# Performance work log

Hardware: AMD Instinct MI355X
Metric: run time of the kernel (lower is better)

The kernel has to match this reference:

```python
import jax, jax.numpy as jnp
import numpy as np

ACT_BITS = 8  # global_act_bit in the original repo
QMAX = float(2 ** ACT_BITS - 1)


def _fake_quant_asym(x):
    """Asymmetric per-tensor fake quantization (weight_quant_fn, activate=True)."""
    mx = jnp.max(x)
    mn = jnp.min(x)
    scale = (mx - mn) / QMAX
    zp = jnp.round(-mn / scale)
    q = jnp.clip(jnp.round(x / scale) + zp, 0.0, QMAX)
    return (q - zp) * scale


def setup_inputs() -> dict:
    key = jax.random.key(0)
    kx, kq, kr, kl, ks = jax.random.split(key, 5)
    B, S, IN, OUT, R = 32, 1024, 1152, 1152, 64
    x = jax.random.normal(kx, (B, S, IN), dtype=jnp.float32)
    quant_w = jax.random.normal(kq, (OUT, IN), dtype=jnp.float32) * 0.02  # quant.weight
    right_w = jax.random.normal(kr, (R, IN), dtype=jnp.float32) * 0.02   # right.weight
    left_w = jax.random.normal(kl, (OUT, R), dtype=jnp.float32) * 0.02   # left.weight
    bias = jnp.zeros((OUT,), dtype=jnp.float32)
    scales = jax.random.uniform(ks, (IN,), dtype=jnp.float32, minval=0.5, maxval=2.0)
    return {"x": x, "quant_w": quant_w, "right_w": right_w,
            "left_w": left_w, "bias": bias, "scales": scales}


def reference(x, quant_w, right_w, left_w, bias, scales):
    # inference path, merge=False: smooth-quant style scale division, then
    # asymmetric per-tensor fake quant, then quant GEMM + low-rank SVD adapter.
    xs = x / scales                                   # [B,S,IN] elementwise
    xq = _fake_quant_asym(xs)                         # global max/min fake quant
    hx = jnp.einsum('bsi,oi->bso', xq, quant_w)       # quantized linear
    lrx = jnp.einsum('bsr,or->bso',
                     jnp.einsum('bsi,ri->bsr', xq, right_w), left_w)  # low-rank
    return hx + lrx + bias
```

## Files before the change

### kernel.cpp

```cpp
#include <hip/hip_runtime.h>
#include <hip/hip_bf16.h>
#include <stdint.h>

#define M_DIM   32768
#define IN_DIM  1152
#define OUT_DIM 1152
#define R_DIM   64
#define QMAXF   255.0f

#define RED_BLOCKS 2048
#define QBLOCKS    4096

typedef float  f32x4  __attribute__((ext_vector_type(4)));
typedef __bf16 bf16x8 __attribute__((ext_vector_type(8)));

static __device__ __forceinline__ unsigned short f2bf(float f) {
    unsigned int u = __float_as_uint(f);
    unsigned int r = (u + 0x7fffu + ((u >> 16) & 1u)) >> 16;
    return (unsigned short)r;
}

__global__ __launch_bounds__(256) void k_wprep(const float* __restrict__ qw,
                                               const float* __restrict__ rw,
                                               const float* __restrict__ lw,
                                               const float* __restrict__ scales,
                                               unsigned short* __restrict__ wc,
                                               float* __restrict__ rs) {
    int idx = blockIdx.x * 256 + threadIdx.x;
    if (idx < IN_DIM) rs[idx] = 1.0f / scales[idx];
    int o = idx / IN_DIM;
    int i = idx - o * IN_DIM;
    float acc = qw[idx];
    #pragma unroll 8
    for (int r = 0; r < R_DIM; r++)
        acc += lw[o * R_DIM + r] * rw[r * IN_DIM + i];
    wc[idx] = f2bf(acc);
}

__global__ __launch_bounds__(256) void k_minmax(const float* __restrict__ x,
                                                const float* __restrict__ rs,
                                                float* __restrict__ partials) {
    const int n4 = (M_DIM * IN_DIM) / 4;
    int tid = blockIdx.x * 256 + threadIdx.x;
    const int stride = RED_BLOCKS * 256;
    float mn = 3.4e38f, mx = -3.4e38f;
    for (int i4 = tid; i4 < n4; i4 += stride) {
        int i = i4 * 4;
        float4 xv = *(const float4*)(x + i);
        int c = i % IN_DIM;
        float4 sv = *(const float4*)(rs + c);
        float a0 = xv.x * sv.x, a1 = xv.y * sv.y;
        float a2 = xv.z * sv.z, a3 = xv.w * sv.w;
        mn = fminf(mn, fminf(fminf(a0, a1), fminf(a2, a3)));
        mx = fmaxf(mx, fmaxf(fmaxf(a0, a1), fmaxf(a2, a3)));
    }
    #pragma unroll
    for (int off = 32; off > 0; off >>= 1) {
        mn = fminf(mn, __shfl_down(mn, off));
        mx = fmaxf(mx, __shfl_down(mx, off));
    }
    __shared__ float smn[4], smx[4];
    int lane = threadIdx.x & 63, wv = threadIdx.x >> 6;
    if (lane == 0) { smn[wv] = mn; smx[wv] = mx; }
    __syncthreads();
    if (threadIdx.x == 0) {
        float bmn = fminf(fminf(smn[0], smn[1]), fminf(smn[2], smn[3]));
        float bmx = fmaxf(fmaxf(smx[0], smx[1]), fmaxf(smx[2], smx[3]));
        partials[blockIdx.x * 2]     = bmn;
        partials[blockIdx.x * 2 + 1] = bmx;
    }
}

__global__ __launch_bounds__(256) void k_finalize(const float* __restrict__ partials,
                                                  const float* __restrict__ scales,
                                                  float* __restrict__ qp,
                                                  float* __restrict__ comb) {
    float mn = 3.4e38f, mx = -3.4e38f;
    for (int i = threadIdx.x; i < RED_BLOCKS; i += 256) {
        mn = fminf(mn, partials[i * 2]);
        mx = fmaxf(mx, partials[i * 2 + 1]);
    }
    #pragma unroll
    for (int off = 32; off > 0; off >>= 1) {
        mn = fminf(mn, __shfl_down(mn, off));
        mx = fmaxf(mx, __shfl_down(mx, off));
    }
    __shared__ float smn[4], smx[4];
    __shared__ float s_qs;
    int lane = threadIdx.x & 63, wv = threadIdx.x >> 6;
    if (lane == 0) { smn[wv] = mn; smx[wv] = mx; }
    __syncthreads();
    if (threadIdx.x == 0) {
        float bmn = fminf(fminf(smn[0], smn[1]), fminf(smn[2], smn[3]));
        float bmx = fmaxf(fmaxf(smx[0], smx[1]), fmaxf(smx[2], smx[3]));
        float qs = (bmx - bmn) / QMAXF;
        float zp = rintf(-bmn / qs);
        qp[0] = qs;
        qp[1] = zp;
        qp[2] = -zp;
        qp[3] = QMAXF - zp;
        s_qs = qs;
    }
    __syncthreads();
    float qs = s_qs;
    for (int c = threadIdx.x; c < IN_DIM; c += 256)
        comb[c] = 1.0f / (scales[c] * qs);
}

__global__ __launch_bounds__(256) void k_quant(const float* __restrict__ x,
                                               const float* __restrict__ comb,
                                               const float* __restrict__ qp,
                                               unsigned short* __restrict__ xq) {
    const float lo = qp[2], hi = qp[3];
    const int n4 = (M_DIM * IN_DIM) / 4;
    int tid = blockIdx.x * 256 + threadIdx.x;
    const int stride = QBLOCKS * 256;
    for (int i4 = tid; i4 < n4; i4 += stride) {
        int i = i4 * 4;
        float4 xv = *(const float4*)(x + i);
        int c = i % IN_DIM;
        float4 cb = *(const float4*)(comb + c);
        float a[4] = { xv.x * cb.x, xv.y * cb.y, xv.z * cb.z, xv.w * cb.w };
        ushort4 o;
        unsigned short* op = (unsigned short*)&o;
        #pragma unroll
        for (int j = 0; j < 4; j++) {
            float q = rintf(a[j]);
            q = fminf(fmaxf(q, lo), hi);
            op[j] = f2bf(q);
        }
        *(ushort4*)(xq + i) = o;
    }
}

#define BM 128
#define BN 128
#define BK 32

__global__ __launch_bounds__(256) void k_gemm(const unsigned short* __restrict__ A,
                                              const unsigned short* __restrict__ Bw,
                                              const float* __restrict__ bias,
                                              const float* __restrict__ qp,
                                              float* __restrict__ C) {
    __shared__ __align__(16) unsigned short As[BM * BK];
    __shared__ __align__(16) unsigned short Bs[BN * BK];
    const int tid = threadIdx.x;
    const int lid = blockIdx.x;
    const int xcd = lid & 7;
    const int kk  = lid >> 3;
    const int bml = kk / 9;
    const int bn  = kk - bml * 9;
    const int bm  = xcd * 32 + bml;
    const int K = IN_DIM, N = OUT_DIM;

    const int r0 = tid >> 2;
    const int c0 = (tid & 3) * 8;
    const unsigned short* ga0 = A  + (size_t)(bm * BM + r0) * K + c0;
    const unsigned short* ga1 = ga0 + (size_t)64 * K;
    const unsigned short* gb0 = Bw + (size_t)(bn * BN + r0) * K + c0;
    const unsigned short* gb1 = gb0 + (size_t)64 * K;
    unsigned short* lA0 = As + tid * 8;
    unsigned short* lA1 = As + tid * 8 + 2048;
    unsigned short* lB0 = Bs + tid * 8;
    unsigned short* lB1 = Bs + tid * 8 + 2048;

    f32x4 acc[4][4];
    #pragma unroll
    for (int mi = 0; mi < 4; mi++)
        #pragma unroll
        for (int ni = 0; ni < 4; ni++)
            acc[mi][ni] = (f32x4)0.0f;

    const int lane = tid & 63, wv = tid >> 6;
    const int wm = (wv & 1) * 64;
    const int wn = (wv >> 1) * 64;
    const int l16 = lane & 15, l4 = lane >> 4;
    const bf16x8* Asv = (const bf16x8*)As;
    const bf16x8* Bsv = (const bf16x8*)Bs;
    const int afo = (wm + l16) * 4 + l4;
    const int bfo = (wn + l16) * 4 + l4;

    for (int k0 = 0; k0 < K; k0 += BK) {
        __builtin_amdgcn_global_load_lds(
            (const __attribute__((address_space(1))) unsigned int*)(ga0 + k0),
            (__attribute__((address_space(3))) unsigned int*)lA0, 16, 0, 0);
        __builtin_amdgcn_global_load_lds(
            (const __attribute__((address_space(1))) unsigned int*)(ga1 + k0),
            (__attribute__((address_space(3))) unsigned int*)lA1, 16, 0, 0);
        __builtin_amdgcn_global_load_lds(
            (const __attribute__((address_space(1))) unsigned int*)(gb0 + k0),
            (__attribute__((address_space(3))) unsigned int*)lB0, 16, 0, 0);
        __builtin_amdgcn_global_load_lds(
            (const __attribute__((address_space(1))) unsigned int*)(gb1 + k0),
            (__attribute__((address_space(3))) unsigned int*)lB1, 16, 0, 0);
        __syncthreads();

        bf16x8 af[4], bf[4];
        #pragma unroll
        for (int mi = 0; mi < 4; mi++) af[mi] = Asv[afo + mi * 64];
        #pragma unroll
        for (int ni = 0; ni < 4; ni++) bf[ni] = Bsv[bfo + ni * 64];
        #pragma unroll
        for (int mi = 0; mi < 4; mi++)
            #pragma unroll
            for (int ni = 0; ni < 4; ni++)
                acc[mi][ni] = __builtin_amdgcn_mfma_f32_16x16x32_bf16(
                    af[mi], bf[ni], acc[mi][ni], 0, 0, 0);
        __syncthreads();
    }

    const float qs = qp[0];
    #pragma unroll
    for (int mi = 0; mi < 4; mi++) {
        int row0 = bm * BM + wm + mi * 16 + l4 * 4;
        #pragma unroll
        for (int ni = 0; ni < 4; ni++) {
            int col = bn * BN + wn + ni * 16 + l16;
            float bv = bias[col];
            #pragma unroll
            for (int r = 0; r < 4; r++)
                C[(size_t)(row0 + r) * N + col] = acc[mi][ni][r] * qs + bv;
        }
    }
}

extern "C" void kernel_launch(void* const* d_in, const int* in_sizes, int n_in,
                              void* d_out, int out_size, void* d_ws, size_t ws_size,
                              hipStream_t stream) {
    const float* x      = (const float*)d_in[0];
    const float* qw     = (const float*)d_in[1];
    const float* rw     = (const float*)d_in[2];
    const float* lw     = (const float*)d_in[3];
    const float* bias   = (const float*)d_in[4];
    const float* scales = (const float*)d_in[5];

    char* ws = (char*)d_ws;
    unsigned short* xq = (unsigned short*)ws;
    unsigned short* wc = (unsigned short*)(ws + 75497472);
    float* partials    = (float*)(ws + 75497472 + 2654208);
    float* qp          = (float*)(ws + 75497472 + 2654208 + 16384);
    float* rs          = (float*)(ws + 75497472 + 2654208 + 16384 + 64);
    float* comb        = (float*)(ws + 75497472 + 2654208 + 16384 + 64 + 4608);

    k_wprep   <<<(OUT_DIM * IN_DIM) / 256, 256, 0, stream>>>(qw, rw, lw, scales, wc, rs);
    k_minmax  <<<RED_BLOCKS, 256, 0, stream>>>(x, rs, partials);
    k_finalize<<<1,          256, 0, stream>>>(partials, scales, qp, comb);
    k_quant   <<<QBLOCKS,    256, 0, stream>>>(x, comb, qp, xq);

    k_gemm<<<2304, 256, 0, stream>>>(xq, wc, bias, qp, (float*)d_out);
}
```

Measured before the change: 419.3 us.

## Fuse fake-quant into GEMM A-tile load and finalize reduction via last-block

The quantize kernel is removed. The GEMM now reads fp32 x directly, applies the scale/round/clamp in registers, and writes bf16 into LDS for the A tile, so the 75MB bf16 xq intermediate is never written or re-read. The separate finalize kernel is folded into the minmax kernel using an atomic counter, with the last block doing the final reduction. The trade-off is that the GEMM re-reads fp32 x (twice the bytes of the old bf16 A) once for each of the 9 N-tiles and redoes the quantization each time. It also loses the async global_load_lds path for A, which may stall the main loop.

```diff
diff --git a/kernel.cpp b/kernel.cpp
--- a/kernel.cpp
+++ b/kernel.cpp
@@ -9,7 +9,6 @@
 #define QMAXF   255.0f
 
 #define RED_BLOCKS 2048
-#define QBLOCKS    4096
 
 typedef float  f32x4  __attribute__((ext_vector_type(4)));
 typedef __bf16 bf16x8 __attribute__((ext_vector_type(8)));
@@ -25,8 +24,10 @@
                                                const float* __restrict__ lw,
                                                const float* __restrict__ scales,
                                                unsigned short* __restrict__ wc,
-                                               float* __restrict__ rs) {
+                                               float* __restrict__ rs,
+                                               unsigned int* __restrict__ cnt) {
     int idx = blockIdx.x * 256 + threadIdx.x;
+    if (idx == 0) *cnt = 0u;
     if (idx < IN_DIM) rs[idx] = 1.0f / scales[idx];
     int o = idx / IN_DIM;
     int i = idx - o * IN_DIM;
@@ -39,7 +40,11 @@
 
 __global__ __launch_bounds__(256) void k_minmax(const float* __restrict__ x,
                                                 const float* __restrict__ rs,
-                                                float* __restrict__ partials) {
+                                                const float* __restrict__ scales,
+                                                float* __restrict__ partials,
+                                                float* __restrict__ qp,
+                                                float* __restrict__ comb,
+                                                unsigned int* __restrict__ cnt) {
     const int n4 = (M_DIM * IN_DIM) / 4;
     int tid = blockIdx.x * 256 + threadIdx.x;
     const int stride = RED_BLOCKS * 256;
@@ -60,32 +65,7 @@
         mx = fmaxf(mx, __shfl_down(mx, off));
     }
     __shared__ float smn[4], smx[4];
-    int lane = threadIdx.x & 63, wv = threadIdx.x >> 6;
-    if (lane == 0) { smn[wv] = mn; smx[wv] = mx; }
-    __syncthreads();
-    if (threadIdx.x == 0) {
-        float bmn = fminf(fminf(smn[0], smn[1]), fminf(smn[2], smn[3]));
-        float bmx = fmaxf(fmaxf(smx[0], smx[1]), fmaxf(smx[2], smx[3]));
-        partials[blockIdx.x * 2]     = bmn;
-        partials[blockIdx.x * 2 + 1] = bmx;
-    }
-}
-
-__global__ __launch_bounds__(256) void k_finalize(const float* __restrict__ partials,
-                                                  const float* __restrict__ scales,
-                                                  float* __restrict__ qp,
-                                                  float* __restrict__ comb) {
-    float mn = 3.4e38f, mx = -3.4e38f;
-    for (int i = threadIdx.x; i < RED_BLOCKS; i += 256) {
-        mn = fminf(mn, partials[i * 2]);
-        mx = fmaxf(mx, partials[i * 2 + 1]);
-    }
-    #pragma unroll
-    for (int off = 32; off > 0; off >>= 1) {
-        mn = fminf(mn, __shfl_down(mn, off));
-        mx = fmaxf(mx, __shfl_down(mx, off));
-    }
-    __shared__ float smn[4], smx[4];
+    __shared__ int sLast;
     __shared__ float s_qs;
     int lane = threadIdx.x & 63, wv = threadIdx.x >> 6;
     if (lane == 0) { smn[wv] = mn; smx[wv] = mx; }
@@ -93,43 +73,47 @@
     if (threadIdx.x == 0) {
         float bmn = fminf(fminf(smn[0], smn[1]), fminf(smn[2], smn[3]));
         float bmx = fmaxf(fmaxf(smx[0], smx[1]), fmaxf(smx[2], smx[3]));
-        float qs = (bmx - bmn) / QMAXF;
-        float zp = rintf(-bmn / qs);
-        qp[0] = qs;
-        qp[1] = zp;
-        qp[2] = -zp;
-        qp[3] = QMAXF - zp;
-        s_qs = qs;
+        __hip_atomic_store(&partials[blockIdx.x * 2],     bmn,
+                           __ATOMIC_RELAXED, __HIP_MEMORY_SCOPE_AGENT);
+        __hip_atomic_store(&partials[blockIdx.x * 2 + 1], bmx,
+                           __ATOMIC_RELAXED, __HIP_MEMORY_SCOPE_AGENT);
+        unsigned int prev = __hip_atomic_fetch_add(cnt, 1u,
+                           __ATOMIC_ACQ_REL, __HIP_MEMORY_SCOPE_AGENT);
+        sLast = (prev == (unsigned int)(RED_BLOCKS - 1));
     }
     __syncthreads();
-    float qs = s_qs;
-    for (int c = threadIdx.x; c < IN_DIM; c += 256)
-        comb[c] = 1.0f / (scales[c] * qs);
-}
-
-__global__ __launch_bounds__(256) void k_quant(const float* __restrict__ x,
-                                               const float* __restrict__ comb,
-                                               const float* __restrict__ qp,
-                                               unsigned short* __restrict__ xq) {
-    const float lo = qp[2], hi = qp[3];
-    const int n4 = (M_DIM * IN_DIM) / 4;
-    int tid = blockIdx.x * 256 + threadIdx.x;
-    const int stride = QBLOCKS * 256;
-    for (int i4 = tid; i4 < n4; i4 += stride) {
-        int i = i4 * 4;
-        float4 xv = *(const float4*)(x + i);
-        int c = i % IN_DIM;
-        float4 cb = *(const float4*)(comb + c);
-        float a[4] = { xv.x * cb.x, xv.y * cb.y, xv.z * cb.z, xv.w * cb.w };
-        ushort4 o;
-        unsigned short* op = (unsigned short*)&o;
-        #pragma unroll
-        for (int j = 0; j < 4; j++) {
-            float q = rintf(a[j]);
-            q = fminf(fmaxf(q, lo), hi);
-            op[j] = f2bf(q);
-        }
-        *(ushort4*)(xq + i) = o;
+    if (sLast) {
+        float fmn = 3.4e38f, fmx = -3.4e38f;
+        for (int i = threadIdx.x; i < RED_BLOCKS; i += 256) {
+            float a = __hip_atomic_load(&partials[i * 2],
+                       __ATOMIC_ACQUIRE, __HIP_MEMORY_SCOPE_AGENT);
+            float b = __hip_atomic_load(&partials[i * 2 + 1],
+                       __ATOMIC_ACQUIRE, __HIP_MEMORY_SCOPE_AGENT);
+            fmn = fminf(fmn, a);
+            fmx = fmaxf(fmx, b);
+        }
+        #pragma unroll
+        for (int off = 32; off > 0; off >>= 1) {
+            fmn = fminf(fmn, __shfl_down(fmn, off));
+            fmx = fmaxf(fmx, __shfl_down(fmx, off));
+        }
+        if (lane == 0) { smn[wv] = fmn; smx[wv] = fmx; }
+        __syncthreads();
+        if (threadIdx.x == 0) {
+            float bmn = fminf(fminf(smn[0], smn[1]), fminf(smn[2], smn[3]));
+            float bmx = fmaxf(fmaxf(smx[0], smx[1]), fmaxf(smx[2], smx[3]));
+            float qs = (bmx - bmn) / QMAXF;
+            float zp = rintf(-bmn / qs);
+            qp[0] = qs;
+            qp[1] = zp;
+            qp[2] = -zp;
+            qp[3] = QMAXF - zp;
+            s_qs = qs;
+        }
+        __syncthreads();
+        float qs = s_qs;
+        for (int c = threadIdx.x; c < IN_DIM; c += 256)
+            comb[c] = 1.0f / (scales[c] * qs);
     }
 }
 
@@ -137,11 +121,12 @@
 #define BN 128
 #define BK 32
 
-__global__ __launch_bounds__(256) void k_gemm(const unsigned short* __restrict__ A,
-                                              const unsigned short* __restrict__ Bw,
-                                              const float* __restrict__ bias,
-                                              const float* __restrict__ qp,
-                                              float* __restrict__ C) {
+__global__ __launch_bounds__(256) void k_gemm_fq(const float* __restrict__ x,
+                                                 const unsigned short* __restrict__ Bw,
+                                                 const float* __restrict__ bias,
+                                                 const float* __restrict__ qp,
+                                                 const float* __restrict__ comb,
+                                                 float* __restrict__ C) {
     __shared__ __align__(16) unsigned short As[BM * BK];
     __shared__ __align__(16) unsigned short Bs[BN * BK];
     const int tid = threadIdx.x;
@@ -153,14 +138,17 @@
     const int bm  = xcd * 32 + bml;
     const int K = IN_DIM, N = OUT_DIM;
 
+    const float lo = qp[2], hi = qp[3];
+
+    const int ar = tid >> 1;
+    const int ac = (tid & 1) * 16;
+    const float* gx = x + (size_t)(bm * BM + ar) * K + ac;
+    unsigned short* lA = As + ar * BK + ac;
+
     const int r0 = tid >> 2;
     const int c0 = (tid & 3) * 8;
-    const unsigned short* ga0 = A  + (size_t)(bm * BM + r0) * K + c0;
-    const unsigned short* ga1 = ga0 + (size_t)64 * K;
     const unsigned short* gb0 = Bw + (size_t)(bn * BN + r0) * K + c0;
     const unsigned short* gb1 = gb0 + (size_t)64 * K;
-    unsigned short* lA0 = As + tid * 8;
-    unsigned short* lA1 = As + tid * 8 + 2048;
     unsigned short* lB0 = Bs + tid * 8;
     unsigned short* lB1 = Bs + tid * 8 + 2048;
 
@@ -182,17 +170,30 @@
 
     for (int k0 = 0; k0 < K; k0 += BK) {
         __builtin_amdgcn_global_load_lds(
-            (const __attribute__((address_space(1))) unsigned int*)(ga0 + k0),
-            (__attribute__((address_space(3))) unsigned int*)lA0, 16, 0, 0);
-        __builtin_amdgcn_global_load_lds(
-            (const __attribute__((address_space(1))) unsigned int*)(ga1 + k0),
-            (__attribute__((address_space(3))) unsigned int*)lA1, 16, 0, 0);
-        __builtin_amdgcn_global_load_lds(
             (const __attribute__((address_space(1))) unsigned int*)(gb0 + k0),
             (__attribute__((address_space(3))) unsigned int*)lB0, 16, 0, 0);
         __builtin_amdgcn_global_load_lds(
             (const __attribute__((address_space(1))) unsigned int*)(gb1 + k0),
             (__attribute__((address_space(3))) unsigned int*)lB1, 16, 0, 0);
+        const float* gxk = gx + k0;
+        const float* cbk = comb + ac + k0;
+        #pragma unroll
+        for (int h = 0; h < 2; h++) {
+            float4 v0 = *(const float4*)(gxk + h * 8);
+            float4 v1 = *(const float4*)(gxk + h * 8 + 4);
+            float4 u0 = *(const float4*)(cbk + h * 8);
+            float4 u1 = *(const float4*)(cbk + h * 8 + 4);
+            bf16x8 o;
+            o[0] = (__bf16)fminf(fmaxf(rintf(v0.x * u0.x), lo), hi);
+            o[1] = (__bf16)fminf(fmaxf(rintf(v0.y * u0.y), lo), hi);
+            o[2] = (__bf16)fminf(fmaxf(rintf(v0.z * u0.z), lo), hi);
+            o[3] = (__bf16)fminf(fmaxf(rintf(v0.w * u0.w), lo), hi);
+            o[4] = (__bf16)fminf(fmaxf(rintf(v1.x * u1.x), lo), hi);
+            o[5] = (__bf16)fminf(fmaxf(rintf(v1.y * u1.y), lo), hi);
+            o[6] = (__bf16)fminf(fmaxf(rintf(v1.z * u1.z), lo), hi);
+            o[7] = (__bf16)fminf(fmaxf(rintf(v1.w * u1.w), lo), hi);
+            *((bf16x8*)lA + h) = o;
+        }
         __syncthreads();
 
         bf16x8 af[4], bf[4];
@@ -235,17 +236,14 @@
     const float* scales = (const float*)d_in[5];
 
     char* ws = (char*)d_ws;
-    unsigned short* xq = (unsigned short*)ws;
-    unsigned short* wc = (unsigned short*)(ws + 75497472);
-    float* partials    = (float*)(ws + 75497472 + 2654208);
-    float* qp          = (float*)(ws + 75497472 + 2654208 + 16384);
-    float* rs          = (float*)(ws + 75497472 + 2654208 + 16384 + 64);
-    float* comb        = (float*)(ws + 75497472 + 2654208 + 16384 + 64 + 4608);
-
-    k_wprep   <<<(OUT_DIM * IN_DIM) / 256, 256, 0, stream>>>(qw, rw, lw, scales, wc, rs);
-    k_minmax  <<<RED_BLOCKS, 256, 0, stream>>>(x, rs, partials);
-    k_finalize<<<1,          256, 0, stream>>>(partials, scales, qp, comb);
-    k_quant   <<<QBLOCKS,    256, 0, stream>>>(x, comb, qp, xq);
-
-    k_gemm<<<2304, 256, 0, stream>>>(xq, wc, bias, qp, (float*)d_out);
-}
+    unsigned short* wc = (unsigned short*)ws;
+    float* partials    = (float*)(ws + 2654208);
+    float* qp          = (float*)(ws + 2654208 + 16384);
+    float* rs          = (float*)(ws + 2654208 + 16384 + 64);
+    float* comb        = (float*)(ws + 2654208 + 16384 + 64 + 4608);
+    unsigned int* cnt  = (unsigned int*)(ws + 2654208 + 16384 + 64 + 4608 + 4608);
+
+    k_wprep <<<(OUT_DIM * IN_DIM) / 256, 256, 0, stream>>>(qw, rw, lw, scales, wc, rs, cnt);
+    k_minmax<<<RED_BLOCKS, 256, 0, stream>>>(x, rs, scales, partials, qp, comb, cnt);
+    k_gemm_fq<<<2304, 256, 0, stream>>>(x, wc, bias, qp, comb, (float*)d_out);
+}
```

After: 521.4 us. 24.3% more time.

## Fuse activation fake-quant into GEMM A-tile loading with double buffering

Applied to the files above, without the earlier changes.

Drops the separate quantization kernel and its bf16 activation buffer. The GEMM now reads fp32 x directly, scales, rounds, clamps and converts to bf16 in registers, then stores the result into a double-buffered LDS A tile. The B tile is also double-buffered, with next-tile loads issued before the current MFMAs. This removes a full write and reread of the quantized activations, but each column block rereads fp32 activations and repeats the quantization arithmetic.

```diff
diff --git a/kernel.cpp b/kernel.cpp
--- a/kernel.cpp
+++ b/kernel.cpp
@@ -9,7 +9,6 @@
 #define QMAXF   255.0f
 
 #define RED_BLOCKS 2048
-#define QBLOCKS    4096
 
 typedef float  f32x4  __attribute__((ext_vector_type(4)));
 typedef __bf16 bf16x8 __attribute__((ext_vector_type(8)));
@@ -107,43 +106,19 @@
         comb[c] = 1.0f / (scales[c] * qs);
 }
 
-__global__ __launch_bounds__(256) void k_quant(const float* __restrict__ x,
-                                               const float* __restrict__ comb,
-                                               const float* __restrict__ qp,
-                                               unsigned short* __restrict__ xq) {
-    const float lo = qp[2], hi = qp[3];
-    const int n4 = (M_DIM * IN_DIM) / 4;
-    int tid = blockIdx.x * 256 + threadIdx.x;
-    const int stride = QBLOCKS * 256;
-    for (int i4 = tid; i4 < n4; i4 += stride) {
-        int i = i4 * 4;
-        float4 xv = *(const float4*)(x + i);
-        int c = i % IN_DIM;
-        float4 cb = *(const float4*)(comb + c);
-        float a[4] = { xv.x * cb.x, xv.y * cb.y, xv.z * cb.z, xv.w * cb.w };
-        ushort4 o;
-        unsigned short* op = (unsigned short*)&o;
-        #pragma unroll
-        for (int j = 0; j < 4; j++) {
-            float q = rintf(a[j]);
-            q = fminf(fmaxf(q, lo), hi);
-            op[j] = f2bf(q);
-        }
-        *(ushort4*)(xq + i) = o;
-    }
-}
-
 #define BM 128
 #define BN 128
 #define BK 32
-
-__global__ __launch_bounds__(256) void k_gemm(const unsigned short* __restrict__ A,
-                                              const unsigned short* __restrict__ Bw,
-                                              const float* __restrict__ bias,
-                                              const float* __restrict__ qp,
-                                              float* __restrict__ C) {
-    __shared__ __align__(16) unsigned short As[BM * BK];
-    __shared__ __align__(16) unsigned short Bs[BN * BK];
+#define NT (IN_DIM / BK)
+
+__global__ __launch_bounds__(256) void k_gemm_fq(const float* __restrict__ x,
+                                                 const unsigned short* __restrict__ Bw,
+                                                 const float* __restrict__ bias,
+                                                 const float* __restrict__ qp,
+                                                 const float* __restrict__ comb,
+                                                 float* __restrict__ C) {
+    __shared__ __align__(16) unsigned short As[2 * BM * BK];
+    __shared__ __align__(16) unsigned short Bs[2 * BN * BK];
     const int tid = threadIdx.x;
     const int lid = blockIdx.x;
     const int xcd = lid & 7;
@@ -153,16 +128,16 @@
     const int bm  = xcd * 32 + bml;
     const int K = IN_DIM, N = OUT_DIM;
 
+    const float lo = qp[2], hi = qp[3];
+
+    const int ar = tid >> 1;
+    const int ac = (tid & 1) * 16;
+    const float* gx = x + (size_t)(bm * BM + ar) * K + ac;
+
     const int r0 = tid >> 2;
     const int c0 = (tid & 3) * 8;
-    const unsigned short* ga0 = A  + (size_t)(bm * BM + r0) * K + c0;
-    const unsigned short* ga1 = ga0 + (size_t)64 * K;
     const unsigned short* gb0 = Bw + (size_t)(bn * BN + r0) * K + c0;
     const unsigned short* gb1 = gb0 + (size_t)64 * K;
-    unsigned short* lA0 = As + tid * 8;
-    unsigned short* lA1 = As + tid * 8 + 2048;
-    unsigned short* lB0 = Bs + tid * 8;
-    unsigned short* lB1 = Bs + tid * 8 + 2048;
 
     f32x4 acc[4][4];
     #pragma unroll
@@ -175,26 +150,74 @@
     const int wm = (wv & 1) * 64;
     const int wn = (wv >> 1) * 64;
     const int l16 = lane & 15, l4 = lane >> 4;
-    const bf16x8* Asv = (const bf16x8*)As;
-    const bf16x8* Bsv = (const bf16x8*)Bs;
     const int afo = (wm + l16) * 4 + l4;
     const int bfo = (wn + l16) * 4 + l4;
 
-    for (int k0 = 0; k0 < K; k0 += BK) {
+    float4 xr0, xr1, xr2, xr3;
+
+    {
         __builtin_amdgcn_global_load_lds(
-            (const __attribute__((address_space(1))) unsigned int*)(ga0 + k0),
-            (__attribute__((address_space(3))) unsigned int*)lA0, 16, 0, 0);
+            (const __attribute__((address_space(1))) unsigned int*)gb0,
+            (__attribute__((address_space(3))) unsigned int*)(Bs + tid * 8), 16, 0, 0);
         __builtin_amdgcn_global_load_lds(
-            (const __attribute__((address_space(1))) unsigned int*)(ga1 + k0),
-            (__attribute__((address_space(3))) unsigned int*)lA1, 16, 0, 0);
-        __builtin_amdgcn_global_load_lds(
-            (const __attribute__((address_space(1))) unsigned int*)(gb0 + k0),
-            (__attribute__((address_space(3))) unsigned int*)lB0, 16, 0, 0);
-        __builtin_amdgcn_global_load_lds(
-            (const __attribute__((address_space(1))) unsigned int*)(gb1 + k0),
-            (__attribute__((address_space(3))) unsigned int*)lB1, 16, 0, 0);
-        __syncthreads();
-
+            (const __attribute__((address_space(1))) unsigned int*)gb1,
+            (__attribute__((address_space(3))) unsigned int*)(Bs + tid * 8 + 2048), 16, 0, 0);
+        xr0 = *(const float4*)(gx + 0);
+        xr1 = *(const float4*)(gx + 4);
+        xr2 = *(const float4*)(gx + 8);
+        xr3 = *(const float4*)(gx + 12);
+        const float* cb = comb + ac;
+        float4 u0 = *(const float4*)(cb + 0);
+        float4 u1 = *(const float4*)(cb + 4);
+        float4 u2 = *(const float4*)(cb + 8);
+        float4 u3 = *(const float4*)(cb + 12);
+        bf16x8 o0, o1;
+        o0[0] = (__bf16)fminf(fmaxf(rintf(xr0.x * u0.x), lo), hi);
+        o0[1] = (__bf16)fminf(fmaxf(rintf(xr0.y * u0.y), lo), hi);
+        o0[2] = (__bf16)fminf(fmaxf(rintf(xr0.z * u0.z), lo), hi);
+        o0[3] = (__bf16)fminf(fmaxf(rintf(xr0.w * u0.w), lo), hi);
+        o0[4] = (__bf16)fminf(fmaxf(rintf(xr1.x * u1.x), lo), hi);
+        o0[5] = (__bf16)fminf(fmaxf(rintf(xr1.y * u1.y), lo), hi);
+        o0[6] = (__bf16)fminf(fmaxf(rintf(xr1.z * u1.z), lo), hi);
+        o0[7] = (__bf16)fminf(fmaxf(rintf(xr1.w * u1.w), lo), hi);
+        o1[0] = (__bf16)fminf(fmaxf(rintf(xr2.x * u2.x), lo), hi);
+        o1[1] = (__bf16)fminf(fmaxf(rintf(xr2.y * u2.y), lo), hi);
+        o1[2] = (__bf16)fminf(fmaxf(rintf(xr2.z * u2.z), lo), hi);
+        o1[3] = (__bf16)fminf(fmaxf(rintf(xr2.w * u2.w), lo), hi);
+        o1[4] = (__bf16)fminf(fmaxf(rintf(xr3.x * u3.x), lo), hi);
+        o1[5] = (__bf16)fminf(fmaxf(rintf(xr3.y * u3.y), lo), hi);
+        o1[6] = (__bf16)fminf(fmaxf(rintf(xr3.z * u3.z), lo), hi);
+        o1[7] = (__bf16)fminf(fmaxf(rintf(xr3.w * u3.w), lo), hi);
+        bf16x8* dst = (bf16x8*)(As + ar * BK + ac);
+        dst[0] = o0;
+        dst[1] = o1;
+    }
+    __syncthreads();
+
+    for (int t = 0; t < NT; ++t) {
+        const int cur = t & 1;
+        const int nxt = cur ^ 1;
+        const bool more = (t + 1) < NT;
+
+        if (more) {
+            const int kc = (t + 1) * BK;
+            __builtin_amdgcn_global_load_lds(
+                (const __attribute__((address_space(1))) unsigned int*)(gb0 + kc),
+                (__attribute__((address_space(3))) unsigned int*)(Bs + nxt * 4096 + tid * 8),
+                16, 0, 0);
+            __builtin_amdgcn_global_load_lds(
+                (const __attribute__((address_space(1))) unsigned int*)(gb1 + kc),
+                (__attribute__((address_space(3))) unsigned int*)(Bs + nxt * 4096 + tid * 8 + 2048),
+                16, 0, 0);
+            const float* gxk = gx + kc;
+            xr0 = *(const float4*)(gxk + 0);
+            xr1 = *(const float4*)(gxk + 4);
+            xr2 = *(const float4*)(gxk + 8);
+            xr3 = *(const float4*)(gxk + 12);
+        }
+
+        const bf16x8* Asv = (const bf16x8*)(As + cur * 4096);
+        const bf16x8* Bsv = (const bf16x8*)(Bs + cur * 4096);
         bf16x8 af[4], bf[4];
         #pragma unroll
         for (int mi = 0; mi < 4; mi++) af[mi] = Asv[afo + mi * 64];
@@ -206,6 +229,35 @@
             for (int ni = 0; ni < 4; ni++)
                 acc[mi][ni] = __builtin_amdgcn_mfma_f32_16x16x32_bf16(
                     af[mi], bf[ni], acc[mi][ni], 0, 0, 0);
+
+        if (more) {
+            const float* cb = comb + ac + (t + 1) * BK;
+            float4 u0 = *(const float4*)(cb + 0);
+            float4 u1 = *(const float4*)(cb + 4);
+            float4 u2 = *(const float4*)(cb + 8);
+            float4 u3 = *(const float4*)(cb + 12);
+            bf16x8 o0, o1;
+            o0[0] = (__bf16)fminf(fmaxf(rintf(xr0.x * u0.x), lo), hi);
+            o0[1] = (__bf16)fminf(fmaxf(rintf(xr0.y * u0.y), lo), hi);
+            o0[2] = (__bf16)fminf(fmaxf(rintf(xr0.z * u0.z), lo), hi);
+            o0[3] = (__bf16)fminf(fmaxf(rintf(xr0.w * u0.w), lo), hi);
+            o0[4] = (__bf16)fminf(fmaxf(rintf(xr1.x * u1.x), lo), hi);
+            o0[5] = (__bf16)fminf(fmaxf(rintf(xr1.y * u1.y), lo), hi);
+            o0[6] = (__bf16)fminf(fmaxf(rintf(xr1.z * u1.z), lo), hi);
+            o0[7] = (__bf16)fminf(fmaxf(rintf(xr1.w * u1.w), lo), hi);
+            o1[0] = (__bf16)fminf(fmaxf(rintf(xr2.x * u2.x), lo), hi);
+            o1[1] = (__bf16)fminf(fmaxf(rintf(xr2.y * u2.y), lo), hi);
+            o1[2] = (__bf16)fminf(fmaxf(rintf(xr2.z * u2.z), lo), hi);
+            o1[3] = (__bf16)fminf(fmaxf(rintf(xr2.w * u2.w), lo), hi);
+            o1[4] = (__bf16)fminf(fmaxf(rintf(xr3.x * u3.x), lo), hi);
+            o1[5] = (__bf16)fminf(fmaxf(rintf(xr3.y * u3.y), lo), hi);
+            o1[6] = (__bf16)fminf(fmaxf(rintf(xr3.z * u3.z), lo), hi);
+            o1[7] = (__bf16)fminf(fmaxf(rintf(xr3.w * u3.w), lo), hi);
+            bf16x8* dst = (bf16x8*)(As + nxt * 4096 + ar * BK + ac);
+            dst[0] = o0;
+            dst[1] = o1;
+        }
+
         __syncthreads();
     }
 
@@ -235,17 +287,15 @@
     const float* scales = (const float*)d_in[5];
 
     char* ws = (char*)d_ws;
-    unsigned short* xq = (unsigned short*)ws;
-    unsigned short* wc = (unsigned short*)(ws + 75497472);
-    float* partials    = (float*)(ws + 75497472 + 2654208);
-    float* qp          = (float*)(ws + 75497472 + 2654208 + 16384);
-    float* rs          = (float*)(ws + 75497472 + 2654208 + 16384 + 64);
-    float* comb        = (float*)(ws + 75497472 + 2654208 + 16384 + 64 + 4608);
+    unsigned short* wc = (unsigned short*)ws;
+    float* partials    = (float*)(ws + 2654208);
+    float* qp          = (float*)(ws + 2654208 + 16384);
+    float* rs          = (float*)(ws + 2654208 + 16384 + 64);
+    float* comb        = (float*)(ws + 2654208 + 16384 + 64 + 4608);
 
     k_wprep   <<<(OUT_DIM * IN_DIM) / 256, 256, 0, stream>>>(qw, rw, lw, scales, wc, rs);
     k_minmax  <<<RED_BLOCKS, 256, 0, stream>>>(x, rs, partials);
     k_finalize<<<1,          256, 0, stream>>>(partials, scales, qp, comb);
-    k_quant   <<<QBLOCKS,    256, 0, stream>>>(x, comb, qp, xq);
-
-    k_gemm<<<2304, 256, 0, stream>>>(xq, wc, bias, qp, (float*)d_out);
-}
+
+    k_gemm_fq<<<2304, 256, 0, stream>>>(x, wc, bias, qp, comb, (float*)d_out);
+}
```

New measurement: 462.3 us. 10.3% more time.

## Fuse weight prep with min/max reduction and fold finalize into quant kernel

Applied to the files above, without the earlier changes.

Merges the weight-combination kernel and the min/max reduction into a single launch, with the block index selecting the role. The reduction now caches reciprocal scales in shared memory. The separate finalize kernel is dropped: every quant block re-reduces the 2048 partials itself and computes the scale inline, which saves two launches and their serialization at the cost of redundant per-block reduction work. The GEMM also drops its XCD-aware block remapping for a plain 2D grid, which may change L2 locality.

```diff
diff --git a/kernel.cpp b/kernel.cpp
--- a/kernel.cpp
+++ b/kernel.cpp
@@ -8,8 +8,9 @@
 #define R_DIM   64
 #define QMAXF   255.0f
 
-#define RED_BLOCKS 2048
-#define QBLOCKS    4096
+#define MM_BLOCKS 2048
+#define WP_BLOCKS (OUT_DIM * IN_DIM / 256)
+#define QBLOCKS   4096
 
 typedef float  f32x4  __attribute__((ext_vector_type(4)));
 typedef __bf16 bf16x8 __attribute__((ext_vector_type(8)));
@@ -20,73 +21,81 @@
     return (unsigned short)r;
 }
 
-__global__ __launch_bounds__(256) void k_wprep(const float* __restrict__ qw,
-                                               const float* __restrict__ rw,
-                                               const float* __restrict__ lw,
-                                               const float* __restrict__ scales,
-                                               unsigned short* __restrict__ wc,
-                                               float* __restrict__ rs) {
-    int idx = blockIdx.x * 256 + threadIdx.x;
-    if (idx < IN_DIM) rs[idx] = 1.0f / scales[idx];
-    int o = idx / IN_DIM;
-    int i = idx - o * IN_DIM;
-    float acc = qw[idx];
-    #pragma unroll 8
-    for (int r = 0; r < R_DIM; r++)
-        acc += lw[o * R_DIM + r] * rw[r * IN_DIM + i];
-    wc[idx] = f2bf(acc);
-}
-
-__global__ __launch_bounds__(256) void k_minmax(const float* __restrict__ x,
+__global__ __launch_bounds__(256) void k_prep(const float* __restrict__ x,
+                                              const float* __restrict__ scales,
+                                              const float* __restrict__ qw,
+                                              const float* __restrict__ rw,
+                                              const float* __restrict__ lw,
+                                              unsigned short* __restrict__ wc,
+                                              float* __restrict__ rs,
+                                              float* __restrict__ partials) {
+    __shared__ __align__(16) float srs[IN_DIM];
+    __shared__ float smn[4], smx[4];
+
+    if (blockIdx.x < MM_BLOCKS) {
+        for (int c = threadIdx.x; c < IN_DIM; c += 256)
+            srs[c] = 1.0f / scales[c];
+        __syncthreads();
+
+        const int n4 = (M_DIM * IN_DIM) / 4;
+        int tid = blockIdx.x * 256 + threadIdx.x;
+        const int stride = MM_BLOCKS * 256;
+        float mn = 3.4e38f, mx = -3.4e38f;
+        for (int i4 = tid; i4 < n4; i4 += stride) {
+            int i = i4 * 4;
+            float4 xv = *(const float4*)(x + i);
+            int c = i % IN_DIM;
+            float4 sv = *(const float4*)(&srs[c]);
+            float a0 = xv.x * sv.x, a1 = xv.y * sv.y;
+            float a2 = xv.z * sv.z, a3 = xv.w * sv.w;
+            mn = fminf(mn, fminf(fminf(a0, a1), fminf(a2, a3)));
+            mx = fmaxf(mx, fmaxf(fmaxf(a0, a1), fmaxf(a2, a3)));
+        }
+        #pragma unroll
+        for (int off = 32; off > 0; off >>= 1) {
+            mn = fminf(mn, __shfl_down(mn, off));
+            mx = fmaxf(mx, __shfl_down(mx, off));
+        }
+        int lane = threadIdx.x & 63, wv = threadIdx.x >> 6;
+        if (lane == 0) { smn[wv] = mn; smx[wv] = mx; }
+        __syncthreads();
+        if (threadIdx.x == 0) {
+            float bmn = fminf(fminf(smn[0], smn[1]), fminf(smn[2], smn[3]));
+            float bmx = fmaxf(fmaxf(smx[0], smx[1]), fmaxf(smx[2], smx[3]));
+            partials[blockIdx.x * 2]     = bmn;
+            partials[blockIdx.x * 2 + 1] = bmx;
+        }
+    } else {
+        int idx = (blockIdx.x - MM_BLOCKS) * 256 + threadIdx.x;
+        if (idx < IN_DIM) rs[idx] = 1.0f / scales[idx];
+        int o = idx / IN_DIM;
+        int i = idx - o * IN_DIM;
+        float acc = qw[idx];
+        #pragma unroll 8
+        for (int r = 0; r < R_DIM; r++)
+            acc += lw[o * R_DIM + r] * rw[r * IN_DIM + i];
+        wc[idx] = f2bf(acc);
+    }
+}
+
+__global__ __launch_bounds__(256) void k_quantf(const float* __restrict__ x,
                                                 const float* __restrict__ rs,
-                                                float* __restrict__ partials) {
-    const int n4 = (M_DIM * IN_DIM) / 4;
-    int tid = blockIdx.x * 256 + threadIdx.x;
-    const int stride = RED_BLOCKS * 256;
+                                                const float* __restrict__ partials,
+                                                float* __restrict__ qp,
+                                                unsigned short* __restrict__ xq) {
+    __shared__ float smn[4], smx[4];
+    __shared__ float s_lo, s_hi, s_rqs;
+
     float mn = 3.4e38f, mx = -3.4e38f;
-    for (int i4 = tid; i4 < n4; i4 += stride) {
-        int i = i4 * 4;
-        float4 xv = *(const float4*)(x + i);
-        int c = i % IN_DIM;
-        float4 sv = *(const float4*)(rs + c);
-        float a0 = xv.x * sv.x, a1 = xv.y * sv.y;
-        float a2 = xv.z * sv.z, a3 = xv.w * sv.w;
-        mn = fminf(mn, fminf(fminf(a0, a1), fminf(a2, a3)));
-        mx = fmaxf(mx, fmaxf(fmaxf(a0, a1), fmaxf(a2, a3)));
+    for (int i = threadIdx.x; i < MM_BLOCKS; i += 256) {
+        mn = fminf(mn, partials[i * 2]);
+        mx = fmaxf(mx, partials[i * 2 + 1]);
     }
     #pragma unroll
     for (int off = 32; off > 0; off >>= 1) {
         mn = fminf(mn, __shfl_down(mn, off));
         mx = fmaxf(mx, __shfl_down(mx, off));
     }
-    __shared__ float smn[4], smx[4];
-    int lane = threadIdx.x & 63, wv = threadIdx.x >> 6;
-    if (lane == 0) { smn[wv] = mn; smx[wv] = mx; }
-    __syncthreads();
-    if (threadIdx.x == 0) {
-        float bmn = fminf(fminf(smn[0], smn[1]), fminf(smn[2], smn[3]));
-        float bmx = fmaxf(fmaxf(smx[0], smx[1]), fmaxf(smx[2], smx[3]));
-        partials[blockIdx.x * 2]     = bmn;
-        partials[blockIdx.x * 2 + 1] = bmx;
-    }
-}
-
-__global__ __launch_bounds__(256) void k_finalize(const float* __restrict__ partials,
-                                                  const float* __restrict__ scales,
-                                                  float* __restrict__ qp,
-                                                  float* __restrict__ comb) {
-    float mn = 3.4e38f, mx = -3.4e38f;
-    for (int i = threadIdx.x; i < RED_BLOCKS; i += 256) {
-        mn = fminf(mn, partials[i * 2]);
-        mx = fmaxf(mx, partials[i * 2 + 1]);
-    }
-    #pragma unroll
-    for (int off = 32; off > 0; off >>= 1) {
-        mn = fminf(mn, __shfl_down(mn, off));
-        mx = fmaxf(mx, __shfl_down(mx, off));
-    }
-    __shared__ float smn[4], smx[4];
-    __shared__ float s_qs;
     int lane = threadIdx.x & 63, wv = threadIdx.x >> 6;
     if (lane == 0) { smn[wv] = mn; smx[wv] = mx; }
     __syncthreads();
@@ -95,23 +104,14 @@
         float bmx = fmaxf(fmaxf(smx[0], smx[1]), fmaxf(smx[2], smx[3]));
         float qs = (bmx - bmn) / QMAXF;
         float zp = rintf(-bmn / qs);
-        qp[0] = qs;
-        qp[1] = zp;
-        qp[2] = -zp;
-        qp[3] = QMAXF - zp;
-        s_qs = qs;
+        s_lo  = -zp;
+        s_hi  = QMAXF - zp;
+        s_rqs = 1.0f / qs;
+        if (blockIdx.x == 0) qp[0] = qs;
     }
     __syncthreads();
-    float qs = s_qs;
-    for (int c = threadIdx.x; c < IN_DIM; c += 256)
-        comb[c] = 1.0f / (scales[c] * qs);
-}
-
-__global__ __launch_bounds__(256) void k_quant(const float* __restrict__ x,
-                                               const float* __restrict__ comb,
-                                               const float* __restrict__ qp,
-                                               unsigned short* __restrict__ xq) {
-    const float lo = qp[2], hi = qp[3];
+    const float lo = s_lo, hi = s_hi, rqs = s_rqs;
+
     const int n4 = (M_DIM * IN_DIM) / 4;
     int tid = blockIdx.x * 256 + threadIdx.x;
     const int stride = QBLOCKS * 256;
@@ -119,8 +119,9 @@
         int i = i4 * 4;
         float4 xv = *(const float4*)(x + i);
         int c = i % IN_DIM;
-        float4 cb = *(const float4*)(comb + c);
-        float a[4] = { xv.x * cb.x, xv.y * cb.y, xv.z * cb.z, xv.w * cb.w };
+        float4 sv = *(const float4*)(rs + c);
+        float a[4] = { (xv.x * sv.x) * rqs, (xv.y * sv.y) * rqs,
+                       (xv.z * sv.z) * rqs, (xv.w * sv.w) * rqs };
         ushort4 o;
         unsigned short* op = (unsigned short*)&o;
         #pragma unroll
@@ -145,12 +146,7 @@
     __shared__ __align__(16) unsigned short As[BM * BK];
     __shared__ __align__(16) unsigned short Bs[BN * BK];
     const int tid = threadIdx.x;
-    const int lid = blockIdx.x;
-    const int xcd = lid & 7;
-    const int kk  = lid >> 3;
-    const int bml = kk / 9;
-    const int bn  = kk - bml * 9;
-    const int bm  = xcd * 32 + bml;
+    const int bm = blockIdx.x, bn = blockIdx.y;
     const int K = IN_DIM, N = OUT_DIM;
 
     const int r0 = tid >> 2;
@@ -240,12 +236,11 @@
     float* partials    = (float*)(ws + 75497472 + 2654208);
     float* qp          = (float*)(ws + 75497472 + 2654208 + 16384);
     float* rs          = (float*)(ws + 75497472 + 2654208 + 16384 + 64);
-    float* comb        = (float*)(ws + 75497472 + 2654208 + 16384 + 64 + 4608);
-
-    k_wprep   <<<(OUT_DIM * IN_DIM) / 256, 256, 0, stream>>>(qw, rw, lw, scales, wc, rs);
-    k_minmax  <<<RED_BLOCKS, 256, 0, stream>>>(x, rs, partials);
-    k_finalize<<<1,          256, 0, stream>>>(partials, scales, qp, comb);
-    k_quant   <<<QBLOCKS,    256, 0, stream>>>(x, comb, qp, xq);
-
-    k_gemm<<<2304, 256, 0, stream>>>(xq, wc, bias, qp, (float*)d_out);
-}
+
+    k_prep  <<<MM_BLOCKS + WP_BLOCKS, 256, 0, stream>>>(x, scales, qw, rw, lw,
+                                                        wc, rs, partials);
+    k_quantf<<<QBLOCKS, 256, 0, stream>>>(x, rs, partials, qp, xq);
+
+    dim3 grid(M_DIM / BM, OUT_DIM / BN);
+    k_gemm<<<grid, 256, 0, stream>>>(xq, wc, bias, qp, (float*)d_out);
+}
```

Measured after the change: 418.1 us. Within noise of the previous version (-0.3%).
